# Kernel tuning notes

Hardware: AMD Instinct MI355X
Metric: run time of the kernel (lower is better)

The kernel has to match this reference:

```python
import jax, jax.numpy as jnp
import numpy as np

K = 4                                   # children per internal node (complete K-ary tree)
L = 7                                   # number of tree levels
N = (K**L - 1) // (K - 1)               # 5461 nodes, BFS order, root = node 0
IN_DIM = 512
MEM_DIM = 512
_STARTS = [(K**l - 1) // (K - 1) for l in range(L + 1)]  # node-index range of each level


def _make_children():
    ch = np.full((N, K), -1, dtype=np.int32)
    for n in range(N):
        base = n * K + 1
        if base + K <= N:                # internal node; leaves keep -1 padding
            ch[n] = np.arange(base, base + K, dtype=np.int32)
    return jnp.asarray(ch)


def setup_inputs() -> dict:
    key = jax.random.key(0)
    ks = jax.random.split(key, 40)
    it = iter(range(1, 40))

    def lin(fin, fout):
        s = 1.0 / np.sqrt(fin)           # torch nn.Linear default init
        W = jax.random.uniform(ks[next(it)], (fin, fout), jnp.float32, -s, s)
        b = jax.random.uniform(ks[next(it)], (fout,), jnp.float32, -s, s)
        return W, b

    inp = {
        "x": jax.random.normal(ks[0], (N, IN_DIM), jnp.float32),
        "children": _make_children(),
    }
    for mod in ("vis", "lang"):
        inp[f"W_ioux_{mod}"], inp[f"b_ioux_{mod}"] = lin(IN_DIM, 3 * MEM_DIM)
        inp[f"W_iouh_{mod}"], inp[f"b_iouh_{mod}"] = lin(MEM_DIM, 3 * MEM_DIM)
        inp[f"W_fx_{mod}"], inp[f"b_fx_{mod}"] = lin(IN_DIM, MEM_DIM)
        inp[f"W_fh_{mod}"], inp[f"b_fh_{mod}"] = lin(MEM_DIM, MEM_DIM)
    inp["W_type"], inp["b_type"] = lin(IN_DIM, 2)
    return inp


def _gates(iou_x, fx_n, W_iouh, b_iouh, W_fh, b_fh, child_c, child_h, h_sum):
    # iou_x: [n,3m] precomputed ioux(x); fx_n: [n,m]; child_*: [n,K,m]; h_sum: [n,m]
    iou = iou_x + h_sum @ W_iouh + b_iouh
    i, o, u = jnp.split(iou, 3, axis=-1)
    f = jax.nn.sigmoid(child_h @ W_fh + b_fh + fx_n[:, None, :])   # [n,K,m]
    c = jax.nn.sigmoid(i) * jnp.tanh(u) + (f * child_c).sum(axis=1)
    h = jax.nn.sigmoid(o) * jnp.tanh(c)
    return c, h


def reference(x, children,
              W_ioux_vis, b_ioux_vis, W_iouh_vis, b_iouh_vis,
              W_fx_vis, b_fx_vis, W_fh_vis, b_fh_vis,
              W_ioux_lang, b_ioux_lang, W_iouh_lang, b_iouh_lang,
              W_fx_lang, b_fx_lang, W_fh_lang, b_fh_lang,
              W_type, b_type):
    dt = x.dtype
    # input-side projections for every node at once (batched GEMMs)
    ioux_v = x @ W_ioux_vis + b_ioux_vis
    fx_v = x @ W_fx_vis + b_fx_vis
    ioux_l = x @ W_ioux_lang + b_ioux_lang
    fx_l = x @ W_fx_lang + b_fx_lang
    # eval-mode greedy type selection: one-hot argmax of type_query logits
    sel_lang = jnp.argmax(x @ W_type + b_type, axis=-1) == 0       # [N] True -> lang branch

    c_all = jnp.zeros((N, MEM_DIM), dt)
    h_all = jnp.zeros((N, MEM_DIM), dt)

    for l in range(L - 1, -1, -1):       # bottom-up over tree levels (static loop)
        s, e = _STARTS[l], _STARTS[l + 1]
        ch = children[s:e]               # [n,K]
        m = (ch >= 0)[..., None].astype(dt)
        idx = jnp.where(ch >= 0, ch, 0)
        child_c = c_all[idx] * m         # leaves: all-zero child states (matches original)
        child_h = h_all[idx] * m
        h_sum = child_h.sum(axis=1)
        c_v, h_v = _gates(ioux_v[s:e], fx_v[s:e], W_iouh_vis, b_iouh_vis,
                          W_fh_vis, b_fh_vis, child_c, child_h, h_sum)
        c_l, h_l = _gates(ioux_l[s:e], fx_l[s:e], W_iouh_lang, b_iouh_lang,
                          W_fh_lang, b_fh_lang, child_c, child_h, h_sum)
        lang = sel_lang[s:e][:, None]
        c_all = c_all.at[s:e].set(jnp.where(lang, c_l, c_v))
        h_all = h_all.at[s:e].set(jnp.where(lang, h_l, h_v))
    return h_all                         # up-state h of every node; root at row 0
```

## Files before the change

### kernel.cpp

```cpp
#include <hip/hip_runtime.h>
#include <cstdint>

constexpr int N_NODES = 5461;

using f16x8 = __attribute__((ext_vector_type(8))) _Float16;
using f32x4 = __attribute__((ext_vector_type(4))) float;

typedef const __attribute__((address_space(1))) unsigned int* gas_p;
typedef __attribute__((address_space(3))) unsigned int* las_p;

__device__ __forceinline__ float sigm(float v) { return 1.0f / (1.0f + __expf(-v)); }

__constant__ int d_STARTS[8] = {0, 1, 5, 21, 85, 341, 1365, 5461};

struct GSet {
    const _Float16 *Ah, *Al;
    const _Float16 *BhL, *BlL, *BhV, *BlV;
    const float *biasL, *biasV;
    float* Y;
    const int* permA;
    int nL, M, Nout;
};

__device__ void gemm_tile(const GSet& S, int tx, int bn)
{
    const int nTl = (S.nL + 127) >> 7;
    int rowBase, rowEnd;
    const _Float16 *Bh, *Bl;
    const float* bias;
    if (tx < nTl) {
        rowBase = tx << 7; rowEnd = S.nL;
        Bh = S.BhL; Bl = S.BlL; bias = S.biasL;
    } else {
        rowBase = S.nL + ((tx - nTl) << 7); rowEnd = S.M;
        Bh = S.BhV; Bl = S.BlV; bias = S.biasV;
    }
    if (rowBase >= rowEnd) return;

    __shared__ _Float16 AsH[2][128 * 32];
    __shared__ _Float16 AsL[2][128 * 32];
    __shared__ _Float16 BsH[2][128 * 32];
    __shared__ _Float16 BsL[2][128 * 32];

    const int tid = threadIdx.x;
    const int wid = tid >> 6;
    const int lane = tid & 63;
    const int wm = (wid >> 2) * 64;
    const int wn = (wid & 3) * 32;
    const int rsel = lane & 15;
    const int kg = lane >> 4;
    const int lrow = lane >> 2;
    const int csrc = ((lane & 3) ^ ((lane >> 3) & 3)) * 8;
    int aR = rowBase + wid * 16 + lrow; if (aR > rowEnd - 1) aR = rowEnd - 1;
    const int a0 = S.permA ? S.permA[aR] : aR;
    const _Float16* gAh = S.Ah + (size_t)a0 * 512 + csrc;
    const _Float16* gAl = S.Al + (size_t)a0 * 512 + csrc;
    const _Float16* gBh = Bh + (size_t)(bn + wid * 16 + lrow) * 512 + csrc;
    const _Float16* gBl = Bl + (size_t)(bn + wid * 16 + lrow) * 512 + csrc;

    f32x4 acc0[4][2] = {};
    f32x4 acc1[4][2] = {};

    auto stage = [&](int k0, int b) {
        __builtin_amdgcn_global_load_lds((gas_p)(const void*)(gAh + k0), (las_p)(void*)(&AsH[b][wid * 512]), 16, 0, 0);
        __builtin_amdgcn_global_load_lds((gas_p)(const void*)(gAl + k0), (las_p)(void*)(&AsL[b][wid * 512]), 16, 0, 0);
        __builtin_amdgcn_global_load_lds((gas_p)(const void*)(gBh + k0), (las_p)(void*)(&BsH[b][wid * 512]), 16, 0, 0);
        __builtin_amdgcn_global_load_lds((gas_p)(const void*)(gBl + k0), (las_p)(void*)(&BsL[b][wid * 512]), 16, 0, 0);
    };

    const int sl = kg ^ ((rsel >> 1) & 3);

    stage(0, 0);
    __syncthreads();
#pragma unroll 1
    for (int step = 0; step < 16; ++step) {
        const int cur = step & 1;
        if (step < 15) stage((step + 1) * 32, cur ^ 1);
        const f16x8* AH = (const f16x8*)AsH[cur];
        const f16x8* AL = (const f16x8*)AsL[cur];
        const f16x8* BH = (const f16x8*)BsH[cur];
        const f16x8* BL = (const f16x8*)BsL[cur];
        f16x8 bh[2], bl[2];
#pragma unroll
        for (int j = 0; j < 2; ++j) {
            int bi = (wn + j * 16 + rsel) * 4 + sl;
            bh[j] = BH[bi];
            bl[j] = BL[bi];
        }
#pragma unroll
        for (int i = 0; i < 4; ++i) {
            int ai = (wm + i * 16 + rsel) * 4 + sl;
            f16x8 ah = AH[ai];
            f16x8 al = AL[ai];
#pragma unroll
            for (int j = 0; j < 2; ++j) {
                acc0[i][j] = __builtin_amdgcn_mfma_f32_16x16x32_f16(ah, bh[j], acc0[i][j], 0, 0, 0);
                acc1[i][j] = __builtin_amdgcn_mfma_f32_16x16x32_f16(ah, bl[j], acc1[i][j], 0, 0, 0);
                acc1[i][j] = __builtin_amdgcn_mfma_f32_16x16x32_f16(al, bh[j], acc1[i][j], 0, 0, 0);
            }
        }
        __syncthreads();
    }

#pragma unroll
    for (int i = 0; i < 4; ++i) {
        int row0 = rowBase + wm + i * 16 + kg * 4;
#pragma unroll
        for (int j = 0; j < 2; ++j) {
            int col = bn + wn + j * 16 + rsel;
            float bb = bias[col];
#pragma unroll
            for (int r = 0; r < 4; ++r) {
                int row = row0 + r;
                if (row < rowEnd)
                    S.Y[(size_t)row * S.Nout + col] = acc0[i][j][r] + acc1[i][j][r] * (1.0f / 2048.0f) + bb;
            }
        }
    }
}

struct GP {
    GSet s0, s1;
    const int* cntPtr;
    int cntScale0, cntScale1;
    int yT0;
};

__global__ __launch_bounds__(512, 4)
void gemm_pair(GP g)
{
    GSet S;
    int bn;
    if (blockIdx.y < (unsigned)g.yT0) {
        S = g.s0; S.nL = g.cntPtr[0] * g.cntScale0;
        bn = blockIdx.y * 128;
    } else {
        S = g.s1; S.nL = g.cntPtr[0] * g.cntScale1;
        bn = (blockIdx.y - g.yT0) * 128;
    }
    gemm_tile(S, blockIdx.x, bn);
}

__device__ __forceinline__ void gbar(int* c, int nb)
{
    __syncthreads();
    if (threadIdx.x == 0) {
        __hip_atomic_fetch_add(c, 1, __ATOMIC_RELEASE, __HIP_MEMORY_SCOPE_AGENT);
        while (__hip_atomic_load(c, __ATOMIC_RELAXED, __HIP_MEMORY_SCOPE_AGENT) < nb)
            __builtin_amdgcn_s_sleep(16);
        int v = __hip_atomic_load(c, __ATOMIC_ACQUIRE, __HIP_MEMORY_SCOPE_AGENT);
        asm volatile("" :: "s"(v));
    }
    __syncthreads();
}

struct Ctx {
    GSet lv0, lv1;
    const int* cnt;
    const float *iou_pre, *fx_pre;
    float *iou_h, *fpre, *c_all, *h_all;
    const int *children, *lvlPerm, *lvlInv, *inv_g;
    const float *b_iouh_v, *b_iouh_l;
    _Float16 *hs_h, *hs_l, *ch_h, *ch_l;
    int* sync;
};

__device__ void combine_body(const Ctx& m, int l, int w, int t, int nw)
{
    const int sPar = d_STARTS[l - 1];
    const int sLvl = d_STARTS[l];
    const int nPar = sLvl - sPar;
    const int d0 = t * 2;
    for (int ip = w; ip < nPar; ip += nw) {
        int p = m.lvlPerm[sPar + ip];
        float hsum[2] = {0.f, 0.f};
#pragma unroll
        for (int k = 0; k < 4; ++k) {
            int cnode = m.children[p * 4 + k];
            int j = m.lvlInv[cnode] - sLvl;
            int u = m.inv_g[cnode];
            size_t ub = (size_t)u * 1536;
            size_t jb = (size_t)j * 1536;
#pragma unroll
            for (int e = 0; e < 2; ++e) {
                int d = d0 + e;
                float iv = m.iou_pre[ub + d]        + m.iou_h[jb + d];
                float ov = m.iou_pre[ub + 512 + d]  + m.iou_h[jb + 512 + d];
                float uv = m.iou_pre[ub + 1024 + d] + m.iou_h[jb + 1024 + d];
                float fxn = m.fx_pre[(size_t)u * 512 + d];
                float csum = 0.f;
#pragma unroll
                for (int k2 = 0; k2 < 4; ++k2) {
                    int gc = m.children[cnode * 4 + k2];
                    float f = sigm(m.fpre[((size_t)(j * 4 + k2)) * 512 + d] + fxn);
                    csum = fmaf(f, m.c_all[(size_t)gc * 512 + d], csum);
                }
                float cc = sigm(iv) * tanhf(uv) + csum;
                float hh = sigm(ov) * tanhf(cc);
                m.c_all[(size_t)cnode * 512 + d] = cc;
                m.h_all[(size_t)cnode * 512 + d] = hh;
                hsum[e] += hh;
                _Float16 hf = (_Float16)hh;
                size_t o = ((size_t)(ip * 4 + k)) * 512 + d;
                m.ch_h[o] = hf;
                m.ch_l[o] = (_Float16)((hh - (float)hf) * 2048.0f);
            }
        }
#pragma unroll
        for (int e = 0; e < 2; ++e) {
            _Float16 sh = (_Float16)hsum[e];
            m.hs_h[(size_t)ip * 512 + d0 + e] = sh;
            m.hs_l[(size_t)ip * 512 + d0 + e] = (_Float16)((hsum[e] - (float)sh) * 2048.0f);
        }
    }
}

__device__ void root_body(const Ctx& m, int w, int t)
{
    if (w >= 2) return;
    int d = w * 256 + t;
    int u = m.inv_g[0];
    size_t ub = (size_t)u * 1536;
    float iv = m.iou_pre[ub + d]        + m.iou_h[d];
    float ov = m.iou_pre[ub + 512 + d]  + m.iou_h[512 + d];
    float uv = m.iou_pre[ub + 1024 + d] + m.iou_h[1024 + d];
    float fxn = m.fx_pre[(size_t)u * 512 + d];
    float csum = 0.f;
#pragma unroll
    for (int k = 0; k < 4; ++k) {
        int gc = m.children[k];
        float f = sigm(m.fpre[(size_t)k * 512 + d] + fxn);
        csum = fmaf(f, m.c_all[(size_t)gc * 512 + d], csum);
    }
    float cc = sigm(iv) * tanhf(uv) + csum;
    float hh = sigm(ov) * tanhf(cc);
    m.c_all[d] = cc;
    m.h_all[d] = hh;
}

__device__ void level_gemm(const Ctx& m, int l, int nb)
{
    const int E = d_STARTS[l + 1] - d_STARTS[l];
    const int langs = m.cnt[1 + l];
    GSet s0 = m.lv0; s0.nL = langs;     s0.M = E;
    GSet s1 = m.lv1; s1.nL = langs * 4; s1.M = E * 4;
    const int gx = (E * 4 + 127) / 128 + 1;
    for (int f = blockIdx.x; f < gx * 16; f += nb) {
        int ty = f & 15, tx = f >> 4;
        if (ty < 12) gemm_tile(s0, tx, ty * 128);
        else         gemm_tile(s1, tx, (ty - 12) * 128);
    }
}

__global__ __launch_bounds__(512, 4)
void tail_mega(Ctx m)
{
    const int nb = gridDim.x;
    const int w = blockIdx.x * 2 + (threadIdx.x >> 8);
    const int t = threadIdx.x & 255;
    const int nw = nb * 2;
    int ph = 0;
#pragma unroll 1
    for (int l = 3; l >= 1; --l) {
        level_gemm(m, l, nb);
        gbar(m.sync + ph, nb); ++ph;
        combine_body(m, l, w, t, nw);
        gbar(m.sync + ph, nb); ++ph;
    }
    level_gemm(m, 0, nb);
    gbar(m.sync + ph, nb);
    root_body(m, w, t);
}

__global__ __launch_bounds__(256)
void combine_gather(int sPar, int sLvl, Ctx m)
{
    int ip = blockIdx.x;
    int p = m.lvlPerm[sPar + ip];
    int t = threadIdx.x;
    int d0 = t * 2;
    float hsum[2] = {0.f, 0.f};
#pragma unroll
    for (int k = 0; k < 4; ++k) {
        int cnode = m.children[p * 4 + k];
        int j = m.lvlInv[cnode] - sLvl;
        int u = m.inv_g[cnode];
        size_t ub = (size_t)u * 1536;
        size_t jb = (size_t)j * 1536;
#pragma unroll
        for (int e = 0; e < 2; ++e) {
            int d = d0 + e;
            float iv = m.iou_pre[ub + d]        + m.iou_h[jb + d];
            float ov = m.iou_pre[ub + 512 + d]  + m.iou_h[jb + 512 + d];
            float uv = m.iou_pre[ub + 1024 + d] + m.iou_h[jb + 1024 + d];
            float fxn = m.fx_pre[(size_t)u * 512 + d];
            float csum = 0.f;
#pragma unroll
            for (int k2 = 0; k2 < 4; ++k2) {
                int gc = m.children[cnode * 4 + k2];
                float f = sigm(m.fpre[((size_t)(j * 4 + k2)) * 512 + d] + fxn);
                csum = fmaf(f, m.c_all[(size_t)gc * 512 + d], csum);
            }
            float cc = sigm(iv) * tanhf(uv) + csum;
            float hh = sigm(ov) * tanhf(cc);
            m.c_all[(size_t)cnode * 512 + d] = cc;
            m.h_all[(size_t)cnode * 512 + d] = hh;
            hsum[e] += hh;
            _Float16 hf = (_Float16)hh;
            size_t o = ((size_t)(ip * 4 + k)) * 512 + d;
            m.ch_h[o] = hf;
            m.ch_l[o] = (_Float16)((hh - (float)hf) * 2048.0f);
        }
    }
#pragma unroll
    for (int e = 0; e < 2; ++e) {
        _Float16 sh = (_Float16)hsum[e];
        m.hs_h[(size_t)ip * 512 + d0 + e] = sh;
        m.hs_l[(size_t)ip * 512 + d0 + e] = (_Float16)((hsum[e] - (float)sh) * 2048.0f);
    }
}

__global__ __launch_bounds__(256)
void leaf_gather(Ctx m)
{
    int ip = blockIdx.x;
    int p = m.lvlPerm[341 + ip];
    int t = threadIdx.x;
    int d0 = t * 2;
    int nLg = m.cnt[0];
    float hsum[2] = {0.f, 0.f};
#pragma unroll
    for (int k = 0; k < 4; ++k) {
        int cnode = m.children[p * 4 + k];
        int u = m.inv_g[cnode];
        const float* bh = (u < nLg) ? m.b_iouh_l : m.b_iouh_v;
        size_t ub = (size_t)u * 1536;
#pragma unroll
        for (int e = 0; e < 2; ++e) {
            int d = d0 + e;
            float iv = m.iou_pre[ub + d]        + bh[d];
            float ov = m.iou_pre[ub + 512 + d]  + bh[512 + d];
            float uv = m.iou_pre[ub + 1024 + d] + bh[1024 + d];
            float cc = sigm(iv) * tanhf(uv);
            float hh = sigm(ov) * tanhf(cc);
            m.c_all[(size_t)cnode * 512 + d] = cc;
            m.h_all[(size_t)cnode * 512 + d] = hh;
            hsum[e] += hh;
            _Float16 hf = (_Float16)hh;
            size_t o = ((size_t)(ip * 4 + k)) * 512 + d;
            m.ch_h[o] = hf;
            m.ch_l[o] = (_Float16)((hh - (float)hf) * 2048.0f);
        }
    }
#pragma unroll
    for (int e = 0; e < 2; ++e) {
        _Float16 sh = (_Float16)hsum[e];
        m.hs_h[(size_t)ip * 512 + d0 + e] = sh;
        m.hs_l[(size_t)ip * 512 + d0 + e] = (_Float16)((hsum[e] - (float)sh) * 2048.0f);
    }
}

__global__ __launch_bounds__(256)
void cast_x_sel(const float* __restrict__ x, const float* __restrict__ Wt,
                const float* __restrict__ bt,
                _Float16* __restrict__ hi, _Float16* __restrict__ lo,
                int* __restrict__ sel)
{
    __shared__ float s0[256], s1[256];
    int t = threadIdx.x;
    int row = blockIdx.x * 2 + (t >> 7);
    int c0 = (t & 127) * 4;
    float p0 = 0.f, p1 = 0.f;
    if (row < N_NODES) {
        size_t off = (size_t)row * 512 + c0;
        float4 v = *(const float4*)(x + off);
        float vv[4] = {v.x, v.y, v.z, v.w};
        union { _Float16 h[4]; ushort4 u; } H, L;
#pragma unroll
        for (int i = 0; i < 4; ++i) {
            _Float16 h = (_Float16)vv[i];
            H.h[i] = h;
            L.h[i] = (_Float16)((vv[i] - (float)h) * 2048.0f);
            p0 = fmaf(vv[i], Wt[(c0 + i) * 2], p0);
            p1 = fmaf(vv[i], Wt[(c0 + i) * 2 + 1], p1);
        }
        *(ushort4*)(hi + off) = H.u;
        *(ushort4*)(lo + off) = L.u;
    }
    s0[t] = p0; s1[t] = p1;
    __syncthreads();
    for (int st = 64; st > 0; st >>= 1) {
        if ((t & 127) < st) { s0[t] += s0[t + st]; s1[t] += s1[t + st]; }
        __syncthreads();
    }
    if ((t & 127) == 0 && row < N_NODES)
        sel[row] = (s0[t] + bt[0] >= s1[t] + bt[1]) ? 1 : 0;
}

struct WtArgs {
    const float* src[8];
    _Float16* dsth[8];
    _Float16* dstl[8];
    int nout[8];
};

__global__ __launch_bounds__(256)
void prep(WtArgs a, const int* __restrict__ sel, int* __restrict__ perm_g,
          int* __restrict__ inv_g, int* __restrict__ lvlPerm,
          int* __restrict__ lvlInv, int* __restrict__ cnt)
{
    if (blockIdx.x < 1536) {
        int idx = blockIdx.x;
        int mi = idx / 192;
        int r = idx % 192;
        int n0 = (r >> 3) * 64;
        int k0 = (r & 7) * 64;
        int Nout = a.nout[mi];
        if (n0 >= Nout) return;
        const float* W = a.src[mi];
        _Float16* TH = a.dsth[mi];
        _Float16* TL = a.dstl[mi];
        __shared__ float tbuf[64][65];
        int tx = threadIdx.x & 63, ty = threadIdx.x >> 6;
#pragma unroll
        for (int rr = ty; rr < 64; rr += 4)
            tbuf[rr][tx] = W[(size_t)(k0 + rr) * Nout + n0 + tx];
        __syncthreads();
#pragma unroll
        for (int rr = ty; rr < 64; rr += 4) {
            float v = tbuf[tx][rr];
            _Float16 h = (_Float16)v;
            TH[(size_t)(n0 + rr) * 512 + k0 + tx] = h;
            TL[(size_t)(n0 + rr) * 512 + k0 + tx] = (_Float16)((v - (float)h) * 2048.0f);
        }
    } else {
        __shared__ int ps[256];
        int b = blockIdx.x - 1536;
        int s, e;
        if (b == 0) { s = 0; e = N_NODES; }
        else { s = d_STARTS[b - 1]; e = d_STARTS[b]; }
        int E = e - s;
        int t = threadIdx.x;
        int chunk = (E + 255) / 256;
        int beg = min(t * chunk, E);
        int end = min(beg + chunk, E);
        int c = 0;
        for (int i = beg; i < end; ++i) c += sel[s + i];
        ps[t] = c;
        __syncthreads();
        for (int off = 1; off < 256; off <<= 1) {
            int other = (t >= off) ? ps[t - off] : 0;
            __syncthreads();
            ps[t] += other;
            __syncthreads();
        }
        int total = ps[255];
        int excl = ps[t] - c;
        int pL = excl;
        int pV = total + (beg - excl);
        for (int i = beg; i < end; ++i) {
            int node = s + i;
            int pos = sel[node] ? pL++ : pV++;
            int slot = s + pos;
            if (b == 0) { perm_g[slot] = node; inv_g[node] = slot; }
            else { lvlPerm[slot] = node; lvlInv[node] = slot; }
        }
        if (t == 0) cnt[b] = total;
    }
}

extern "C" void kernel_launch(void* const* d_in, const int* in_sizes, int n_in,
                              void* d_out, int out_size, void* d_ws, size_t ws_size,
                              hipStream_t stream)
{
    const float* x        = (const float*)d_in[0];
    const int*   children = (const int*)  d_in[1];
    const float* W_ioux_v = (const float*)d_in[2];
    const float* b_ioux_v = (const float*)d_in[3];
    const float* W_iouh_v = (const float*)d_in[4];
    const float* b_iouh_v = (const float*)d_in[5];
    const float* W_fx_v   = (const float*)d_in[6];
    const float* b_fx_v   = (const float*)d_in[7];
    const float* W_fh_v   = (const float*)d_in[8];
    const float* b_fh_v   = (const float*)d_in[9];
    const float* W_ioux_l = (const float*)d_in[10];
    const float* b_ioux_l = (const float*)d_in[11];
    const float* W_iouh_l = (const float*)d_in[12];
    const float* b_iouh_l = (const float*)d_in[13];
    const float* W_fx_l   = (const float*)d_in[14];
    const float* b_fx_l   = (const float*)d_in[15];
    const float* W_fh_l   = (const float*)d_in[16];
    const float* b_fh_l   = (const float*)d_in[17];
    const float* W_type   = (const float*)d_in[18];
    const float* b_type   = (const float*)d_in[19];
    float* h_all = (float*)d_out;

    float* p = (float*)d_ws;
    float* iou_pre = p; p += (size_t)N_NODES * 1536;
    float* fx_pre  = p; p += (size_t)N_NODES * 512;
    float* c_all   = p; p += (size_t)N_NODES * 512;
    float* iou_h   = p; p += (size_t)1024 * 1536;
    float* fpre    = p; p += (size_t)4096 * 512;
    int* sel     = (int*)p; p += 6144;
    int* perm_g  = (int*)p; p += 6144;
    int* inv_g   = (int*)p; p += 6144;
    int* lvlPerm = (int*)p; p += 2048;
    int* lvlInv  = (int*)p; p += 2048;
    int* cnt     = (int*)p; p += 64;
    int* gsync   = (int*)p; p += 64;
    _Float16* q = (_Float16*)p;
    _Float16* xh   = q; q += (size_t)N_NODES * 512;
    _Float16* xl   = q; q += (size_t)N_NODES * 512;
    _Float16* hs_h = q; q += (size_t)1024 * 512;
    _Float16* hs_l = q; q += (size_t)1024 * 512;
    _Float16* ch_h = q; q += (size_t)4096 * 512;
    _Float16* ch_l = q; q += (size_t)4096 * 512;
    _Float16* wt_ioux_vh = q; q += (size_t)1536 * 512;
    _Float16* wt_ioux_vl = q; q += (size_t)1536 * 512;
    _Float16* wt_ioux_lh = q; q += (size_t)1536 * 512;
    _Float16* wt_ioux_ll = q; q += (size_t)1536 * 512;
    _Float16* wt_iouh_vh = q; q += (size_t)1536 * 512;
    _Float16* wt_iouh_vl = q; q += (size_t)1536 * 512;
    _Float16* wt_iouh_lh = q; q += (size_t)1536 * 512;
    _Float16* wt_iouh_ll = q; q += (size_t)1536 * 512;
    _Float16* wt_fx_vh   = q; q += (size_t)512 * 512;
    _Float16* wt_fx_vl   = q; q += (size_t)512 * 512;
    _Float16* wt_fx_lh   = q; q += (size_t)512 * 512;
    _Float16* wt_fx_ll   = q; q += (size_t)512 * 512;
    _Float16* wt_fh_vh   = q; q += (size_t)512 * 512;
    _Float16* wt_fh_vl   = q; q += (size_t)512 * 512;
    _Float16* wt_fh_lh   = q; q += (size_t)512 * 512;
    _Float16* wt_fh_ll   = q; q += (size_t)512 * 512;

    hipMemsetAsync(gsync, 0, 64 * sizeof(int), stream);

    cast_x_sel<<<(N_NODES + 1) / 2, 256, 0, stream>>>(x, W_type, b_type, xh, xl, sel);

    WtArgs wa;
    wa.src[0] = W_ioux_v; wa.dsth[0] = wt_ioux_vh; wa.dstl[0] = wt_ioux_vl; wa.nout[0] = 1536;
    wa.src[1] = W_ioux_l; wa.dsth[1] = wt_ioux_lh; wa.dstl[1] = wt_ioux_ll; wa.nout[1] = 1536;
    wa.src[2] = W_iouh_v; wa.dsth[2] = wt_iouh_vh; wa.dstl[2] = wt_iouh_vl; wa.nout[2] = 1536;
    wa.src[3] = W_iouh_l; wa.dsth[3] = wt_iouh_lh; wa.dstl[3] = wt_iouh_ll; wa.nout[3] = 1536;
    wa.src[4] = W_fx_v;   wa.dsth[4] = wt_fx_vh;   wa.dstl[4] = wt_fx_vl;   wa.nout[4] = 512;
    wa.src[5] = W_fx_l;   wa.dsth[5] = wt_fx_lh;   wa.dstl[5] = wt_fx_ll;   wa.nout[5] = 512;
    wa.src[6] = W_fh_v;   wa.dsth[6] = wt_fh_vh;   wa.dstl[6] = wt_fh_vl;   wa.nout[6] = 512;
    wa.src[7] = W_fh_l;   wa.dsth[7] = wt_fh_lh;   wa.dstl[7] = wt_fh_ll;   wa.nout[7] = 512;
    prep<<<1543, 256, 0, stream>>>(wa, sel, perm_g, inv_g, lvlPerm, lvlInv, cnt);

    Ctx m{};
    m.lv0 = GSet{hs_h, hs_l, wt_iouh_lh, wt_iouh_ll, wt_iouh_vh, wt_iouh_vl,
                 b_iouh_l, b_iouh_v, iou_h, nullptr, 0, 0, 1536};
    m.lv1 = GSet{ch_h, ch_l, wt_fh_lh, wt_fh_ll, wt_fh_vh, wt_fh_vl,
                 b_fh_l, b_fh_v, fpre, nullptr, 0, 0, 512};
    m.cnt = cnt;
    m.iou_pre = iou_pre; m.fx_pre = fx_pre;
    m.iou_h = iou_h; m.fpre = fpre; m.c_all = c_all; m.h_all = h_all;
    m.children = children; m.lvlPerm = lvlPerm; m.lvlInv = lvlInv; m.inv_g = inv_g;
    m.b_iouh_v = b_iouh_v; m.b_iouh_l = b_iouh_l;
    m.hs_h = hs_h; m.hs_l = hs_l; m.ch_h = ch_h; m.ch_l = ch_l;
    m.sync = gsync;

    {
        GP g{};
        g.s0 = GSet{xh, xl, wt_ioux_lh, wt_ioux_ll, wt_ioux_vh, wt_ioux_vl,
                    b_ioux_l, b_ioux_v, iou_pre, perm_g, 0, N_NODES, 1536};
        g.s1 = GSet{xh, xl, wt_fx_lh, wt_fx_ll, wt_fx_vh, wt_fx_vl,
                    b_fx_l, b_fx_v, fx_pre, perm_g, 0, N_NODES, 512};
        g.cntPtr = cnt; g.cntScale0 = 1; g.cntScale1 = 1; g.yT0 = 12;
        gemm_pair<<<dim3(44, 16), 512, 0, stream>>>(g);
    }

    leaf_gather<<<1024, 256, 0, stream>>>(m);

    static const int STARTS[8] = {0, 1, 5, 21, 85, 341, 1365, 5461};
    for (int l = 5; l >= 4; --l) {
        int s = STARTS[l];
        int E = STARTS[l + 1] - s;
        GP g{};
        g.s0 = m.lv0; g.s0.M = E;
        g.s1 = m.lv1; g.s1.M = E * 4;
        g.cntPtr = cnt + 1 + l; g.cntScale0 = 1; g.cntScale1 = 4; g.yT0 = 12;
        int gx = (E * 4 + 127) / 128 + 1;
        gemm_pair<<<dim3(gx, 16), 512, 0, stream>>>(g);
        combine_gather<<<STARTS[l] - STARTS[l - 1], 256, 0, stream>>>(STARTS[l - 1], s, m);
    }

    tail_mega<<<48, 512, 0, stream>>>(m);
}
```

Baseline: 280.9 us.

## Replace grid-barrier tail megakernel with per-level per-node GEMV combine kernels

```diff
diff --git a/kernel.cpp b/kernel.cpp
--- a/kernel.cpp
+++ b/kernel.cpp
@@ -141,19 +141,6 @@
     gemm_tile(S, blockIdx.x, bn);
 }
 
-__device__ __forceinline__ void gbar(int* c, int nb)
-{
-    __syncthreads();
-    if (threadIdx.x == 0) {
-        __hip_atomic_fetch_add(c, 1, __ATOMIC_RELEASE, __HIP_MEMORY_SCOPE_AGENT);
-        while (__hip_atomic_load(c, __ATOMIC_RELAXED, __HIP_MEMORY_SCOPE_AGENT) < nb)
-            __builtin_amdgcn_s_sleep(16);
-        int v = __hip_atomic_load(c, __ATOMIC_ACQUIRE, __HIP_MEMORY_SCOPE_AGENT);
-        asm volatile("" :: "s"(v));
-    }
-    __syncthreads();
-}
-
 struct Ctx {
     GSet lv0, lv1;
     const int* cnt;
@@ -162,115 +149,7 @@
     const int *children, *lvlPerm, *lvlInv, *inv_g;
     const float *b_iouh_v, *b_iouh_l;
     _Float16 *hs_h, *hs_l, *ch_h, *ch_l;
-    int* sync;
 };
-
-__device__ void combine_body(const Ctx& m, int l, int w, int t, int nw)
-{
-    const int sPar = d_STARTS[l - 1];
-    const int sLvl = d_STARTS[l];
-    const int nPar = sLvl - sPar;
-    const int d0 = t * 2;
-    for (int ip = w; ip < nPar; ip += nw) {
-        int p = m.lvlPerm[sPar + ip];
-        float hsum[2] = {0.f, 0.f};
-#pragma unroll
-        for (int k = 0; k < 4; ++k) {
-            int cnode = m.children[p * 4 + k];
-            int j = m.lvlInv[cnode] - sLvl;
-            int u = m.inv_g[cnode];
-            size_t ub = (size_t)u * 1536;
-            size_t jb = (size_t)j * 1536;
-#pragma unroll
-            for (int e = 0; e < 2; ++e) {
-                int d = d0 + e;
-                float iv = m.iou_pre[ub + d]        + m.iou_h[jb + d];
-                float ov = m.iou_pre[ub + 512 + d]  + m.iou_h[jb + 512 + d];
-                float uv = m.iou_pre[ub + 1024 + d] + m.iou_h[jb + 1024 + d];
-                float fxn = m.fx_pre[(size_t)u * 512 + d];
-                float csum = 0.f;
-#pragma unroll
-                for (int k2 = 0; k2 < 4; ++k2) {
-                    int gc = m.children[cnode * 4 + k2];
-                    float f = sigm(m.fpre[((size_t)(j * 4 + k2)) * 512 + d] + fxn);
-                    csum = fmaf(f, m.c_all[(size_t)gc * 512 + d], csum);
-                }
-                float cc = sigm(iv) * tanhf(uv) + csum;
-                float hh = sigm(ov) * tanhf(cc);
-                m.c_all[(size_t)cnode * 512 + d] = cc;
-                m.h_all[(size_t)cnode * 512 + d] = hh;
-                hsum[e] += hh;
-                _Float16 hf = (_Float16)hh;
-                size_t o = ((size_t)(ip * 4 + k)) * 512 + d;
-                m.ch_h[o] = hf;
-                m.ch_l[o] = (_Float16)((hh - (float)hf) * 2048.0f);
-            }
-        }
-#pragma unroll
-        for (int e = 0; e < 2; ++e) {
-            _Float16 sh = (_Float16)hsum[e];
-            m.hs_h[(size_t)ip * 512 + d0 + e] = sh;
-            m.hs_l[(size_t)ip * 512 + d0 + e] = (_Float16)((hsum[e] - (float)sh) * 2048.0f);
-        }
-    }
-}
-
-__device__ void root_body(const Ctx& m, int w, int t)
-{
-    if (w >= 2) return;
-    int d = w * 256 + t;
-    int u = m.inv_g[0];
-    size_t ub = (size_t)u * 1536;
-    float iv = m.iou_pre[ub + d]        + m.iou_h[d];
-    float ov = m.iou_pre[ub + 512 + d]  + m.iou_h[512 + d];
-    float uv = m.iou_pre[ub + 1024 + d] + m.iou_h[1024 + d];
-    float fxn = m.fx_pre[(size_t)u * 512 + d];
-    float csum = 0.f;
-#pragma unroll
-    for (int k = 0; k < 4; ++k) {
-        int gc = m.children[k];
-        float f = sigm(m.fpre[(size_t)k * 512 + d] + fxn);
-        csum = fmaf(f, m.c_all[(size_t)gc * 512 + d], csum);
-    }
-    float cc = sigm(iv) * tanhf(uv) + csum;
-    float hh = sigm(ov) * tanhf(cc);
-    m.c_all[d] = cc;
-    m.h_all[d] = hh;
-}
-
-__device__ void level_gemm(const Ctx& m, int l, int nb)
-{
-    const int E = d_STARTS[l + 1] - d_STARTS[l];
-    const int langs = m.cnt[1 + l];
-    GSet s0 = m.lv0; s0.nL = langs;     s0.M = E;
-    GSet s1 = m.lv1; s1.nL = langs * 4; s1.M = E * 4;
-    const int gx = (E * 4 + 127) / 128 + 1;
-    for (int f = blockIdx.x; f < gx * 16; f += nb) {
-        int ty = f & 15, tx = f >> 4;
-        if (ty < 12) gemm_tile(s0, tx, ty * 128);
-        else         gemm_tile(s1, tx, (ty - 12) * 128);
-    }
-}
-
-__global__ __launch_bounds__(512, 4)
-void tail_mega(Ctx m)
-{
-    const int nb = gridDim.x;
-    const int w = blockIdx.x * 2 + (threadIdx.x >> 8);
-    const int t = threadIdx.x & 255;
-    const int nw = nb * 2;
-    int ph = 0;
-#pragma unroll 1
-    for (int l = 3; l >= 1; --l) {
-        level_gemm(m, l, nb);
-        gbar(m.sync + ph, nb); ++ph;
-        combine_body(m, l, w, t, nw);
-        gbar(m.sync + ph, nb); ++ph;
-    }
-    level_gemm(m, 0, nb);
-    gbar(m.sync + ph, nb);
-    root_body(m, w, t);
-}
 
 __global__ __launch_bounds__(256)
 void combine_gather(int sPar, int sLvl, Ctx m)
@@ -358,6 +237,96 @@
         m.hs_h[(size_t)ip * 512 + d0 + e] = sh;
         m.hs_l[(size_t)ip * 512 + d0 + e] = (_Float16)((hsum[e] - (float)sh) * 2048.0f);
     }
+}
+
+struct GV {
+    const float *iou_pre, *fx_pre;
+    float *c_all, *h_all;
+    const int *children, *inv_g;
+    const int* cnt;
+    const _Float16 *WiouhHl, *WiouhLl, *WiouhHv, *WiouhLv;
+    const _Float16 *WfhHl, *WfhLl, *WfhHv, *WfhLv;
+    const float *b_iouh_l, *b_iouh_v, *b_fh_l, *b_fh_v;
+};
+
+__global__ __launch_bounds__(512, 2)
+void gemv_combine(int s, GV g)
+{
+    __shared__ float hsL[512];
+    __shared__ float chL[4][512];
+    __shared__ float cL[4][512];
+    __shared__ float douts[3584];
+    const int n = s + blockIdx.x;
+    const int t = threadIdx.x;
+    const int u = g.inv_g[n];
+    const bool lang = u < g.cnt[0];
+
+    int cn[4];
+#pragma unroll
+    for (int k = 0; k < 4; ++k) cn[k] = g.children[n * 4 + k];
+    float hsv = 0.f;
+#pragma unroll
+    for (int k = 0; k < 4; ++k) {
+        float hv = g.h_all[(size_t)cn[k] * 512 + t];
+        chL[k][t] = hv;
+        hsv += hv;
+        cL[k][t] = g.c_all[(size_t)cn[k] * 512 + t];
+    }
+    hsL[t] = hsv;
+    __syncthreads();
+
+    const _Float16* WHi = lang ? g.WiouhHl : g.WiouhHv;
+    const _Float16* WLi = lang ? g.WiouhLl : g.WiouhLv;
+    const _Float16* WHf = lang ? g.WfhHl   : g.WfhHv;
+    const _Float16* WLf = lang ? g.WfhLl   : g.WfhLv;
+
+#pragma unroll
+    for (int i = 0; i < 7; ++i) {
+        const int o = i * 512 + t;
+        const float* a;
+        const _Float16 *bh, *bl;
+        if (i < 3) {
+            a = hsL;
+            bh = WHi + (size_t)o * 512;
+            bl = WLi + (size_t)o * 512;
+        } else {
+            a = chL[i - 3];
+            bh = WHf + (size_t)t * 512;
+            bl = WLf + (size_t)t * 512;
+        }
+        float accH = 0.f, accL = 0.f;
+#pragma unroll 4
+        for (int d = 0; d < 512; d += 8) {
+            f16x8 vh = *(const f16x8*)(bh + d);
+            f16x8 vl = *(const f16x8*)(bl + d);
+#pragma unroll
+            for (int j = 0; j < 8; ++j) {
+                float av = a[d + j];
+                accH = fmaf(av, (float)vh[j], accH);
+                accL = fmaf(av, (float)vl[j], accL);
+            }
+        }
+        douts[o] = accH + accL * (1.0f / 2048.0f);
+    }
+    __syncthreads();
+
+    const float* b_iouh = lang ? g.b_iouh_l : g.b_iouh_v;
+    const float* b_fh   = lang ? g.b_fh_l   : g.b_fh_v;
+    size_t ub = (size_t)u * 1536;
+    float iv = g.iou_pre[ub + t]        + douts[t]        + b_iouh[t];
+    float ov = g.iou_pre[ub + 512 + t]  + douts[512 + t]  + b_iouh[512 + t];
+    float uv = g.iou_pre[ub + 1024 + t] + douts[1024 + t] + b_iouh[1024 + t];
+    float fxn = g.fx_pre[(size_t)u * 512 + t] + b_fh[t];
+    float csum = 0.f;
+#pragma unroll
+    for (int k = 0; k < 4; ++k) {
+        float f = sigm(douts[1536 + k * 512 + t] + fxn);
+        csum = fmaf(f, cL[k][t], csum);
+    }
+    float cc = sigm(iv) * tanhf(uv) + csum;
+    float hh = sigm(ov) * tanhf(cc);
+    g.c_all[(size_t)n * 512 + t] = cc;
+    g.h_all[(size_t)n * 512 + t] = hh;
 }
 
 __global__ __launch_bounds__(256)
@@ -507,7 +476,6 @@
     int* lvlPerm = (int*)p; p += 2048;
     int* lvlInv  = (int*)p; p += 2048;
     int* cnt     = (int*)p; p += 64;
-    int* gsync   = (int*)p; p += 64;
     _Float16* q = (_Float16*)p;
     _Float16* xh   = q; q += (size_t)N_NODES * 512;
     _Float16* xl   = q; q += (size_t)N_NODES * 512;
@@ -532,8 +500,6 @@
     _Float16* wt_fh_lh   = q; q += (size_t)512 * 512;
     _Float16* wt_fh_ll   = q; q += (size_t)512 * 512;
 
-    hipMemsetAsync(gsync, 0, 64 * sizeof(int), stream);
-
     cast_x_sel<<<(N_NODES + 1) / 2, 256, 0, stream>>>(x, W_type, b_type, xh, xl, sel);
 
     WtArgs wa;
@@ -558,7 +524,6 @@
     m.children = children; m.lvlPerm = lvlPerm; m.lvlInv = lvlInv; m.inv_g = inv_g;
     m.b_iouh_v = b_iouh_v; m.b_iouh_l = b_iouh_l;
     m.hs_h = hs_h; m.hs_l = hs_l; m.ch_h = ch_h; m.ch_l = ch_l;
-    m.sync = gsync;
 
     {
         GP g{};
@@ -585,5 +550,19 @@
         combine_gather<<<STARTS[l] - STARTS[l - 1], 256, 0, stream>>>(STARTS[l - 1], s, m);
     }
 
-    tail_mega<<<48, 512, 0, stream>>>(m);
-}
+    GV gv{};
+    gv.iou_pre = iou_pre; gv.fx_pre = fx_pre;
+    gv.c_all = c_all; gv.h_all = h_all;
+    gv.children = children; gv.inv_g = inv_g; gv.cnt = cnt;
+    gv.WiouhHl = wt_iouh_lh; gv.WiouhLl = wt_iouh_ll;
+    gv.WiouhHv = wt_iouh_vh; gv.WiouhLv = wt_iouh_vl;
+    gv.WfhHl = wt_fh_lh; gv.WfhLl = wt_fh_ll;
+    gv.WfhHv = wt_fh_vh; gv.WfhLv = wt_fh_vl;
+    gv.b_iouh_l = b_iouh_l; gv.b_iouh_v = b_iouh_v;
+    gv.b_fh_l = b_fh_l; gv.b_fh_v = b_fh_v;
+    for (int l = 3; l >= 0; --l) {
+        int s = STARTS[l];
+        int E = STARTS[l + 1] - s;
+        gemv_combine<<<E, 512, 0, stream>>>(s, gv);
+    }
+}
```

After: 1.053 ms. 3.75x slower.
